# Optimization experiments

Hardware: AMD Instinct MI355X
Metric: run time of the kernel (lower is better)

## Reference

```python
import jax, jax.numpy as jnp
import numpy as np

N_NODES = 50000
N_EDGES = 1600000
IN_DIM = 128
HEADS = 8
OUT_C = 16  # per-head channels; HEADS*OUT_C == IN_DIM -> residual active
NEG_SLOPE = 0.2
BN_EPS = 1e-5


def setup_inputs() -> dict:
    key = jax.random.key(0)
    ks = jax.random.split(key, 8)
    x = jax.random.normal(ks[0], (N_NODES, IN_DIM), dtype=jnp.float32)
    edge_index = jax.random.randint(ks[1], (2, N_EDGES), 0, N_NODES, dtype=jnp.int64)
    # GATConv params (PyG: shared lin for src/dst on single-tensor input)
    W = jax.random.normal(ks[2], (IN_DIM, HEADS * OUT_C), dtype=jnp.float32) / np.sqrt(IN_DIM)
    att_src = jax.random.normal(ks[3], (HEADS, OUT_C), dtype=jnp.float32) / np.sqrt(OUT_C)
    att_dst = jax.random.normal(ks[4], (HEADS, OUT_C), dtype=jnp.float32) / np.sqrt(OUT_C)
    bias = jnp.zeros((HEADS * OUT_C,), dtype=jnp.float32)
    # BatchNorm1d affine params
    gamma = jnp.ones((HEADS * OUT_C,), dtype=jnp.float32)
    beta = jnp.zeros((HEADS * OUT_C,), dtype=jnp.float32)
    return {"x": x, "edge_index": edge_index, "W": W, "att_src": att_src,
            "att_dst": att_dst, "bias": bias, "gamma": gamma, "beta": beta}


def reference(x, edge_index, W, att_src, att_dst, bias, gamma, beta):
    N = x.shape[0]
    H, C = att_src.shape
    src, dst = edge_index[0], edge_index[1]

    xl = (x @ W).reshape(N, H, C)                      # [N,H,C]
    a_src = jnp.sum(xl * att_src[None], axis=-1)       # [N,H]
    a_dst = jnp.sum(xl * att_dst[None], axis=-1)       # [N,H]

    e = jax.nn.leaky_relu(a_src[src] + a_dst[dst], NEG_SLOPE)  # [E,H]
    # segment softmax over incoming edges of each dst node
    m = jax.ops.segment_max(e, dst, num_segments=N)    # [N,H], -inf for empty
    m = jnp.where(jnp.isfinite(m), m, 0.0)
    ex = jnp.exp(e - m[dst])                           # [E,H]
    denom = jax.ops.segment_sum(ex, dst, num_segments=N)
    alpha = ex / (denom[dst] + 1e-16)                  # [E,H]

    out = jax.ops.segment_sum(alpha[:, :, None] * xl[src], dst, num_segments=N)  # [N,H,C]
    h = out.reshape(N, H * C) + bias

    # BatchNorm1d (training mode: batch statistics, biased variance)
    mean = jnp.mean(h, axis=0)
    var = jnp.mean((h - mean) ** 2, axis=0)
    h = (h - mean) * jax.lax.rsqrt(var + BN_EPS) * gamma + beta

    h = jax.nn.relu(h)
    return x + h  # residual (in_dim == H*C)
```

## Files before the change

kernel.cpp:

```cpp
#include <hip/hip_runtime.h>
#include <hip/hip_fp16.h>
#include <math.h>

#define N_NODES 50000
#define N_EDGES 1600000
#define DIM 128
#define HEADS 8
#define NEG_SLOPE 0.2f
#define BN_EPS 1e-5f

typedef _Float16 f16x8 __attribute__((ext_vector_type(8)));
typedef float f32x4 __attribute__((ext_vector_type(4)));

#define NBUCK 196
#define SEGCAP 12288
#define CHUNK 8192
#define NB_A ((N_EDGES + CHUNK - 1) / CHUNK)
#define LIN_NB ((N_NODES + 127) / 128)
#define LIN_K1 195
#define LIN_K2 (LIN_NB - LIN_K1)
#define P1_NB (NB_A + LIN_K1)
#define P2_NB (NBUCK + LIN_K2)

struct BinAShm {
    int hist[NBUCK], excl[NBUCK], cnt2[NBUCK];
    int sc[256];
    unsigned int buf[CHUNK];
};
struct BinBShm {
    int la[256], ea[256];
    int hist[256], excl[256], cnt2[256], sc[256];
    unsigned short out[SEGCAP];
};
struct LinShm { __half wh[16384]; };

__device__ __forceinline__ void lin_block(
        int linb, const float* __restrict__ x, const float* __restrict__ W,
        const float* __restrict__ att_s, const float* __restrict__ att_d,
        __half* __restrict__ xlh, float* __restrict__ a_src,
        float* __restrict__ a_dst, __half* wh) {
    const int t = threadIdx.x;
    for (int v = t; v < 2048; v += 512) {
        const int g = v >> 6, lane = v & 63;
        const int nt = g >> 2, kt = g & 3;
        const int q = lane >> 4, n = lane & 15;
        #pragma unroll
        for (int j = 0; j < 8; ++j)
            wh[(size_t)(g * 64 + lane) * 8 + j] =
                __float2half(W[(kt * 32 + q * 8 + j) * DIM + nt * 16 + n]);
    }
    __syncthreads();

    const int wave = t >> 6;
    const int lane = t & 63;
    const int q = lane >> 4, n = lane & 15;
    const int nb = (linb * 8 + wave) * 16;

    const int rowA = min(nb + n, N_NODES - 1);
    const float* xr = x + (size_t)rowA * DIM;
    f16x8 a[4];
    #pragma unroll
    for (int kt = 0; kt < 4; ++kt) {
        const float4 p0 = *(const float4*)(xr + kt * 32 + q * 8);
        const float4 p1 = *(const float4*)(xr + kt * 32 + q * 8 + 4);
        a[kt][0] = (_Float16)p0.x; a[kt][1] = (_Float16)p0.y;
        a[kt][2] = (_Float16)p0.z; a[kt][3] = (_Float16)p0.w;
        a[kt][4] = (_Float16)p1.x; a[kt][5] = (_Float16)p1.y;
        a[kt][6] = (_Float16)p1.z; a[kt][7] = (_Float16)p1.w;
    }

    f32x4 acc[8];
    #pragma unroll
    for (int nt = 0; nt < 8; ++nt) acc[nt] = (f32x4){0.f, 0.f, 0.f, 0.f};

    const f16x8* wb = (const f16x8*)wh;
    #pragma unroll
    for (int nt = 0; nt < 8; ++nt) {
        #pragma unroll
        for (int kt = 0; kt < 4; ++kt) {
            const f16x8 b = wb[(nt * 4 + kt) * 64 + lane];
            acc[nt] = __builtin_amdgcn_mfma_f32_16x16x32_f16(a[kt], b, acc[nt], 0, 0, 0);
        }
    }

    const int r0 = nb + q * 4;
    #pragma unroll
    for (int nt = 0; nt < 8; ++nt) {
        const float as = att_s[nt * 16 + n];
        const float ad = att_d[nt * 16 + n];
        #pragma unroll
        for (int r = 0; r < 4; ++r) {
            const int row = r0 + r;
            const float v = acc[nt][r];
            float s = v * as;
            float d = v * ad;
            #pragma unroll
            for (int off = 8; off; off >>= 1) {
                s += __shfl_xor(s, off, 16);
                d += __shfl_xor(d, off, 16);
            }
            if (row < N_NODES) {
                xlh[(size_t)row * DIM + nt * 16 + n] = __float2half(v);
                if (n == 0) {
                    a_src[row * HEADS + nt] = s * 1.44269504f;
                    a_dst[row * HEADS + nt] = d * 1.44269504f;
                }
            }
        }
    }
}

__global__ __launch_bounds__(512) void k_phase1(
        const float* __restrict__ x, const float* __restrict__ W,
        const float* __restrict__ att_s, const float* __restrict__ att_d,
        const int* __restrict__ ei, unsigned int* __restrict__ meta,
        unsigned int* __restrict__ pairs, __half* __restrict__ xlh,
        float* __restrict__ a_src, float* __restrict__ a_dst) {
    __shared__ union { BinAShm a; LinShm l; } sh;
    const int t = threadIdx.x;

    if (blockIdx.x < NB_A) {
        const int blk = blockIdx.x;
        const int base = blk * CHUNK;
        const int cnt = min(CHUNK, N_EDGES - base);

        if (t < NBUCK) { sh.a.hist[t] = 0; sh.a.cnt2[t] = 0; }
        __syncthreads();
        for (int i = t * 4; i < cnt; i += 2048) {
            const int4 dv = *(const int4*)(ei + N_EDGES + base + i);
            atomicAdd(&sh.a.hist[dv.x >> 8], 1);
            atomicAdd(&sh.a.hist[dv.y >> 8], 1);
            atomicAdd(&sh.a.hist[dv.z >> 8], 1);
            atomicAdd(&sh.a.hist[dv.w >> 8], 1);
        }
        __syncthreads();
        if (t < 256) sh.a.sc[t] = (t < NBUCK) ? sh.a.hist[t] : 0;
        __syncthreads();
        for (int d = 1; d < 256; d <<= 1) {
            int xo = 0;
            if (t < 256 && t >= d) xo = sh.a.sc[t - d];
            __syncthreads();
            if (t < 256) sh.a.sc[t] += xo;
            __syncthreads();
        }
        if (t < NBUCK) {
            const int ex = sh.a.sc[t] - sh.a.hist[t];
            sh.a.excl[t] = ex;
            meta[(size_t)blk * NBUCK + t] =
                (unsigned int)sh.a.hist[t] | ((unsigned int)ex << 16);
        }
        __syncthreads();
        for (int i = t * 4; i < cnt; i += 2048) {
            const int4 sv = *(const int4*)(ei + base + i);
            const int4 dv = *(const int4*)(ei + N_EDGES + base + i);
            const int ss[4] = {sv.x, sv.y, sv.z, sv.w};
            const int dd[4] = {dv.x, dv.y, dv.z, dv.w};
            #pragma unroll
            for (int k = 0; k < 4; ++k) {
                const int b = dd[k] >> 8;
                const int r = atomicAdd(&sh.a.cnt2[b], 1);
                sh.a.buf[sh.a.excl[b] + r] = (unsigned int)ss[k]
                    | ((unsigned int)(dd[k] & 255) << 16);
            }
        }
        __syncthreads();
        for (int i = t * 4; i < cnt; i += 2048)
            *(int4*)(pairs + base + i) = *(const int4*)(sh.a.buf + i);
    } else {
        lin_block(blockIdx.x - NB_A, x, W, att_s, att_d, xlh, a_src, a_dst, sh.l.wh);
    }
}

__global__ __launch_bounds__(512) void k_phase2(
        const unsigned int* __restrict__ pairs, const unsigned int* __restrict__ meta,
        unsigned short* __restrict__ csr, int2* __restrict__ nrange,
        float* __restrict__ gsums,
        const float* __restrict__ x, const float* __restrict__ W,
        const float* __restrict__ att_s, const float* __restrict__ att_d,
        __half* __restrict__ xlh, float* __restrict__ a_src,
        float* __restrict__ a_dst) {
    __shared__ union { BinBShm b; LinShm l; } sh;
    const int t = threadIdx.x;

    if (blockIdx.x < NBUCK) {
        const int b = blockIdx.x;
        if (b == 0 && t < 256) gsums[t] = 0.f;

        if (t < 256) {
            int len = 0, off = 0;
            if (t < NB_A) {
                const unsigned int m = meta[(size_t)t * NBUCK + b];
                len = (int)(m & 0xFFFF);
                off = (int)(m >> 16);
            }
            sh.b.la[t] = len; sh.b.ea[t] = off;
            sh.b.hist[t] = 0; sh.b.cnt2[t] = 0;
        }
        __syncthreads();

        const int wave = t >> 6, lane = t & 63;

        for (int r = wave; r < NB_A; r += 8) {
            const int len = sh.b.la[r];
            const unsigned int* src = pairs + (size_t)r * CHUNK + sh.b.ea[r];
            for (int j = lane; j < len; j += 64)
                atomicAdd(&sh.b.hist[(src[j] >> 16) & 255], 1);
        }
        __syncthreads();
        if (t < 256) sh.b.sc[t] = sh.b.hist[t];
        __syncthreads();
        for (int d = 1; d < 256; d <<= 1) {
            int xo = 0;
            if (t < 256 && t >= d) xo = sh.b.sc[t - d];
            __syncthreads();
            if (t < 256) sh.b.sc[t] += xo;
            __syncthreads();
        }
        if (t < 256) {
            sh.b.excl[t] = sh.b.sc[t] - sh.b.hist[t];
            const int node = (b << 8) + t;
            if (node < N_NODES) {
                int2 rg;
                rg.x = b * SEGCAP + sh.b.excl[t];
                rg.y = rg.x + sh.b.hist[t];
                nrange[node] = rg;
            }
        }
        __syncthreads();
        const int cnt = sh.b.sc[255];

        for (int r = wave; r < NB_A; r += 8) {
            const int len = sh.b.la[r];
            const unsigned int* src = pairs + (size_t)r * CHUNK + sh.b.ea[r];
            for (int j = lane; j < len; j += 64) {
                const unsigned int u = src[j];
                const int dl = (u >> 16) & 255;
                const int p = atomicAdd(&sh.b.cnt2[dl], 1);
                sh.b.out[sh.b.excl[dl] + p] = (unsigned short)(u & 0xFFFF);
            }
        }
        __syncthreads();
        for (int i = t; i < cnt; i += 512)
            csr[(size_t)b * SEGCAP + i] = sh.b.out[i];
    } else {
        lin_block(LIN_K1 + (int)blockIdx.x - NBUCK, x, W, att_s, att_d,
                  xlh, a_src, a_dst, sh.l.wh);
    }
}

#define AGG_NB (N_NODES / 4)

__global__ void k_aggr9(const int2* __restrict__ nrange,
                        const unsigned short* __restrict__ csr,
                        const float* __restrict__ a_src, const float* __restrict__ a_dst,
                        const __half* __restrict__ xlh, float* __restrict__ y) {
    const int d = blockIdx.x * 4 + (threadIdx.x >> 6);
    const int lane = threadIdx.x & 63;
    const int g = lane >> 4;
    const int cl = lane & 15;
    const int h = cl >> 1;
    const int2 rg = nrange[d];
    const int lo = rg.x, hi = rg.y;
    const float ad = a_dst[d * HEADS + h];

    float acc[8];
    #pragma unroll
    for (int k = 0; k < 8; ++k) acc[k] = 0.f;
    float dsum = 0.f;

    int i = lo;
    for (; i + 16 <= hi; i += 16) {
        const int s0 = csr[i + g];
        const int s1 = csr[i + 4 + g];
        const int s2 = csr[i + 8 + g];
        const int s3 = csr[i + 12 + g];
        const float as0 = a_src[s0 * HEADS + h];
        const float as1 = a_src[s1 * HEADS + h];
        const float as2 = a_src[s2 * HEADS + h];
        const float as3 = a_src[s3 * HEADS + h];
        const f16x8 x0 = *(const f16x8*)(xlh + (size_t)s0 * DIM + cl * 8);
        const f16x8 x1 = *(const f16x8*)(xlh + (size_t)s1 * DIM + cl * 8);
        const f16x8 x2 = *(const f16x8*)(xlh + (size_t)s2 * DIM + cl * 8);
        const f16x8 x3 = *(const f16x8*)(xlh + (size_t)s3 * DIM + cl * 8);
        const float e0 = as0 + ad;
        const float e1 = as1 + ad;
        const float e2 = as2 + ad;
        const float e3 = as3 + ad;
        const float w0 = exp2f(fmaxf(e0, NEG_SLOPE * e0));
        const float w1 = exp2f(fmaxf(e1, NEG_SLOPE * e1));
        const float w2 = exp2f(fmaxf(e2, NEG_SLOPE * e2));
        const float w3 = exp2f(fmaxf(e3, NEG_SLOPE * e3));
        dsum += (w0 + w1) + (w2 + w3);
        #pragma unroll
        for (int k = 0; k < 8; ++k) acc[k] = fmaf(w0, (float)x0[k], acc[k]);
        #pragma unroll
        for (int k = 0; k < 8; ++k) acc[k] = fmaf(w1, (float)x1[k], acc[k]);
        #pragma unroll
        for (int k = 0; k < 8; ++k) acc[k] = fmaf(w2, (float)x2[k], acc[k]);
        #pragma unroll
        for (int k = 0; k < 8; ++k) acc[k] = fmaf(w3, (float)x3[k], acc[k]);
    }
    for (; i + 8 <= hi; i += 8) {
        const int s0 = csr[i + g];
        const int s1 = csr[i + 4 + g];
        const float as0 = a_src[s0 * HEADS + h];
        const float as1 = a_src[s1 * HEADS + h];
        const f16x8 x0 = *(const f16x8*)(xlh + (size_t)s0 * DIM + cl * 8);
        const f16x8 x1 = *(const f16x8*)(xlh + (size_t)s1 * DIM + cl * 8);
        const float e0 = as0 + ad;
        const float e1 = as1 + ad;
        const float w0 = exp2f(fmaxf(e0, NEG_SLOPE * e0));
        const float w1 = exp2f(fmaxf(e1, NEG_SLOPE * e1));
        dsum += w0 + w1;
        #pragma unroll
        for (int k = 0; k < 8; ++k) acc[k] = fmaf(w0, (float)x0[k], acc[k]);
        #pragma unroll
        for (int k = 0; k < 8; ++k) acc[k] = fmaf(w1, (float)x1[k], acc[k]);
    }
    for (; i < hi; i += 4) {
        const int idx = i + g;
        const int sv = csr[min(idx, hi - 1)];
        const float e = a_src[sv * HEADS + h] + ad;
        const f16x8 xv = *(const f16x8*)(xlh + (size_t)sv * DIM + cl * 8);
        float w = exp2f(fmaxf(e, NEG_SLOPE * e));
        if (idx >= hi) w = 0.f;
        dsum += w;
        #pragma unroll
        for (int k = 0; k < 8; ++k) acc[k] = fmaf(w, (float)xv[k], acc[k]);
    }
    #pragma unroll
    for (int k = 0; k < 8; ++k) {
        acc[k] += __shfl_xor(acc[k], 16);
        acc[k] += __shfl_xor(acc[k], 32);
    }
    dsum += __shfl_xor(dsum, 16);
    dsum += __shfl_xor(dsum, 32);
    const float inv = 1.f / (dsum + 1e-16f);
    float2 o;
    o.x = acc[2 * g] * inv;
    o.y = acc[2 * g + 1] * inv;
    *(float2*)(y + (size_t)d * DIM + cl * 8 + g * 2) = o;
}

__global__ void k_stats(const float* __restrict__ y, const float* __restrict__ bias,
                        float* __restrict__ gsums) {
    const int c = threadIdx.x;
    const float b = bias[c];
    float s = 0.f, ss = 0.f;
    for (int n = blockIdx.x; n < N_NODES; n += gridDim.x) {
        const float h = y[n * DIM + c] + b;
        s += h;
        ss += h * h;
    }
    atomicAdd(&gsums[c], s);
    atomicAdd(&gsums[DIM + c], ss);
}

__global__ void k_final(float* __restrict__ y, const float* __restrict__ x,
                        const float* __restrict__ sums, const float* __restrict__ sumsq,
                        const float* __restrict__ gamma, const float* __restrict__ beta,
                        const float* __restrict__ bias) {
    const int q = blockIdx.x * blockDim.x + threadIdx.x;
    const int cq = q & (DIM / 4 - 1);
    const float4 sm = ((const float4*)sums)[cq];
    const float4 sq = ((const float4*)sumsq)[cq];
    const float4 gm = ((const float4*)gamma)[cq];
    const float4 bt = ((const float4*)beta)[cq];
    const float4 bs = ((const float4*)bias)[cq];
    float4 v = ((const float4*)y)[q];
    const float4 xv = ((const float4*)x)[q];
    const float inv_n = 1.f / (float)N_NODES;
#define BNC(c) { const float mean = sm.c * inv_n;                         \
                 const float var = sq.c * inv_n - mean * mean;            \
                 const float sc = rsqrtf(var + BN_EPS) * gm.c;            \
                 const float sh = bt.c + (bs.c - mean) * sc;              \
                 v.c = xv.c + fmaxf(v.c * sc + sh, 0.f); }
    BNC(x) BNC(y) BNC(z) BNC(w)
#undef BNC
    ((float4*)y)[q] = v;
}

extern "C" void kernel_launch(void* const* d_in, const int* in_sizes, int n_in,
                              void* d_out, int out_size, void* d_ws, size_t ws_size,
                              hipStream_t stream) {
    const float* x     = (const float*)d_in[0];
    const int*   ei    = (const int*)  d_in[1];
    const float* W     = (const float*)d_in[2];
    const float* att_s = (const float*)d_in[3];
    const float* att_d = (const float*)d_in[4];
    const float* bias  = (const float*)d_in[5];
    const float* gamma = (const float*)d_in[6];
    const float* beta  = (const float*)d_in[7];
    float* y = (float*)d_out;

    __half* xlh  = (__half*)d_ws;
    float* a_src = (float*)(xlh + (size_t)N_NODES * DIM);
    float* a_dst = a_src + (size_t)N_NODES * HEADS;
    float* sums  = a_dst + (size_t)N_NODES * HEADS;
    float* sumsq = sums  + DIM;
    int2*  nrange = (int2*)(sumsq + DIM);
    unsigned int* meta  = (unsigned int*)(nrange + N_NODES);
    unsigned int* pairs = meta + (size_t)NB_A * NBUCK;
    unsigned short* csr = (unsigned short*)(pairs + (size_t)NB_A * CHUNK);

    k_phase1<<<P1_NB, 512, 0, stream>>>(x, W, att_s, att_d, ei, meta, pairs,
                                        xlh, a_src, a_dst);
    k_phase2<<<P2_NB, 512, 0, stream>>>(pairs, meta, csr, nrange, sums,
                                        x, W, att_s, att_d, xlh, a_src, a_dst);
    k_aggr9<<<AGG_NB, 256, 0, stream>>>(nrange, csr, a_src, a_dst, xlh, y);
    k_stats<<<512, DIM, 0, stream>>>(y, bias, sums);
    k_final<<<(size_t)N_NODES * DIM / 4 / 256, 256, 0, stream>>>(y, x, sums, sumsq,
                                                                 gamma, beta, bias);
}
```

Baseline: 234.1 us.

## Fuse second-pass binning with aggregation into one kernel using 128-node buckets

```diff
diff --git a/kernel.cpp b/kernel.cpp
--- a/kernel.cpp
+++ b/kernel.cpp
@@ -12,25 +12,17 @@
 typedef _Float16 f16x8 __attribute__((ext_vector_type(8)));
 typedef float f32x4 __attribute__((ext_vector_type(4)));
 
-#define NBUCK 196
-#define SEGCAP 12288
+#define NBUCK 391
+#define BSEGCAP 4864
 #define CHUNK 8192
 #define NB_A ((N_EDGES + CHUNK - 1) / CHUNK)
 #define LIN_NB ((N_NODES + 127) / 128)
-#define LIN_K1 195
-#define LIN_K2 (LIN_NB - LIN_K1)
-#define P1_NB (NB_A + LIN_K1)
-#define P2_NB (NBUCK + LIN_K2)
+#define P1_NB (NB_A + LIN_NB)
 
 struct BinAShm {
     int hist[NBUCK], excl[NBUCK], cnt2[NBUCK];
-    int sc[256];
+    int sc[512];
     unsigned int buf[CHUNK];
-};
-struct BinBShm {
-    int la[256], ea[256];
-    int hist[256], excl[256], cnt2[256], sc[256];
-    unsigned short out[SEGCAP];
 };
 struct LinShm { __half wh[16384]; };
 
@@ -124,23 +116,23 @@
         const int base = blk * CHUNK;
         const int cnt = min(CHUNK, N_EDGES - base);
 
-        if (t < NBUCK) { sh.a.hist[t] = 0; sh.a.cnt2[t] = 0; }
+        for (int j = t; j < NBUCK; j += 512) { sh.a.hist[j] = 0; sh.a.cnt2[j] = 0; }
         __syncthreads();
         for (int i = t * 4; i < cnt; i += 2048) {
             const int4 dv = *(const int4*)(ei + N_EDGES + base + i);
-            atomicAdd(&sh.a.hist[dv.x >> 8], 1);
-            atomicAdd(&sh.a.hist[dv.y >> 8], 1);
-            atomicAdd(&sh.a.hist[dv.z >> 8], 1);
-            atomicAdd(&sh.a.hist[dv.w >> 8], 1);
-        }
-        __syncthreads();
-        if (t < 256) sh.a.sc[t] = (t < NBUCK) ? sh.a.hist[t] : 0;
-        __syncthreads();
-        for (int d = 1; d < 256; d <<= 1) {
+            atomicAdd(&sh.a.hist[dv.x >> 7], 1);
+            atomicAdd(&sh.a.hist[dv.y >> 7], 1);
+            atomicAdd(&sh.a.hist[dv.z >> 7], 1);
+            atomicAdd(&sh.a.hist[dv.w >> 7], 1);
+        }
+        __syncthreads();
+        sh.a.sc[t] = (t < NBUCK) ? sh.a.hist[t] : 0;
+        __syncthreads();
+        for (int d = 1; d < 512; d <<= 1) {
             int xo = 0;
-            if (t < 256 && t >= d) xo = sh.a.sc[t - d];
+            if (t >= d) xo = sh.a.sc[t - d];
             __syncthreads();
-            if (t < 256) sh.a.sc[t] += xo;
+            sh.a.sc[t] += xo;
             __syncthreads();
         }
         if (t < NBUCK) {
@@ -157,10 +149,10 @@
             const int dd[4] = {dv.x, dv.y, dv.z, dv.w};
             #pragma unroll
             for (int k = 0; k < 4; ++k) {
-                const int b = dd[k] >> 8;
+                const int b = dd[k] >> 7;
                 const int r = atomicAdd(&sh.a.cnt2[b], 1);
                 sh.a.buf[sh.a.excl[b] + r] = (unsigned int)ss[k]
-                    | ((unsigned int)(dd[k] & 255) << 16);
+                    | ((unsigned int)(dd[k] & 127) << 16);
             }
         }
         __syncthreads();
@@ -171,175 +163,149 @@
     }
 }
 
-__global__ __launch_bounds__(512) void k_phase2(
+__global__ __launch_bounds__(1024) void k_binaggr(
         const unsigned int* __restrict__ pairs, const unsigned int* __restrict__ meta,
-        unsigned short* __restrict__ csr, int2* __restrict__ nrange,
-        float* __restrict__ gsums,
-        const float* __restrict__ x, const float* __restrict__ W,
-        const float* __restrict__ att_s, const float* __restrict__ att_d,
-        __half* __restrict__ xlh, float* __restrict__ a_src,
-        float* __restrict__ a_dst) {
-    __shared__ union { BinBShm b; LinShm l; } sh;
+        const float* __restrict__ a_src, const float* __restrict__ a_dst,
+        const __half* __restrict__ xlh, float* __restrict__ y,
+        float* __restrict__ gsums) {
+    __shared__ int la[NB_A], ea[NB_A];
+    __shared__ int hist[128], excl[128], cnt2[128], sc[128];
+    __shared__ unsigned short out[BSEGCAP];
     const int t = threadIdx.x;
-
-    if (blockIdx.x < NBUCK) {
-        const int b = blockIdx.x;
-        if (b == 0 && t < 256) gsums[t] = 0.f;
-
-        if (t < 256) {
-            int len = 0, off = 0;
-            if (t < NB_A) {
-                const unsigned int m = meta[(size_t)t * NBUCK + b];
-                len = (int)(m & 0xFFFF);
-                off = (int)(m >> 16);
-            }
-            sh.b.la[t] = len; sh.b.ea[t] = off;
-            sh.b.hist[t] = 0; sh.b.cnt2[t] = 0;
-        }
-        __syncthreads();
-
-        const int wave = t >> 6, lane = t & 63;
-
-        for (int r = wave; r < NB_A; r += 8) {
-            const int len = sh.b.la[r];
-            const unsigned int* src = pairs + (size_t)r * CHUNK + sh.b.ea[r];
-            for (int j = lane; j < len; j += 64)
-                atomicAdd(&sh.b.hist[(src[j] >> 16) & 255], 1);
-        }
-        __syncthreads();
-        if (t < 256) sh.b.sc[t] = sh.b.hist[t];
-        __syncthreads();
-        for (int d = 1; d < 256; d <<= 1) {
-            int xo = 0;
-            if (t < 256 && t >= d) xo = sh.b.sc[t - d];
-            __syncthreads();
-            if (t < 256) sh.b.sc[t] += xo;
-            __syncthreads();
-        }
-        if (t < 256) {
-            sh.b.excl[t] = sh.b.sc[t] - sh.b.hist[t];
-            const int node = (b << 8) + t;
-            if (node < N_NODES) {
-                int2 rg;
-                rg.x = b * SEGCAP + sh.b.excl[t];
-                rg.y = rg.x + sh.b.hist[t];
-                nrange[node] = rg;
-            }
-        }
-        __syncthreads();
-        const int cnt = sh.b.sc[255];
-
-        for (int r = wave; r < NB_A; r += 8) {
-            const int len = sh.b.la[r];
-            const unsigned int* src = pairs + (size_t)r * CHUNK + sh.b.ea[r];
-            for (int j = lane; j < len; j += 64) {
-                const unsigned int u = src[j];
-                const int dl = (u >> 16) & 255;
-                const int p = atomicAdd(&sh.b.cnt2[dl], 1);
-                sh.b.out[sh.b.excl[dl] + p] = (unsigned short)(u & 0xFFFF);
-            }
-        }
-        __syncthreads();
-        for (int i = t; i < cnt; i += 512)
-            csr[(size_t)b * SEGCAP + i] = sh.b.out[i];
-    } else {
-        lin_block(LIN_K1 + (int)blockIdx.x - NBUCK, x, W, att_s, att_d,
-                  xlh, a_src, a_dst, sh.l.wh);
-    }
-}
-
-#define AGG_NB (N_NODES / 4)
-
-__global__ void k_aggr9(const int2* __restrict__ nrange,
-                        const unsigned short* __restrict__ csr,
-                        const float* __restrict__ a_src, const float* __restrict__ a_dst,
-                        const __half* __restrict__ xlh, float* __restrict__ y) {
-    const int d = blockIdx.x * 4 + (threadIdx.x >> 6);
-    const int lane = threadIdx.x & 63;
+    const int b = blockIdx.x;
+    if (b == 0 && t < 256) gsums[t] = 0.f;
+
+    if (t < NB_A) {
+        const unsigned int m = meta[(size_t)t * NBUCK + b];
+        la[t] = (int)(m & 0xFFFF);
+        ea[t] = (int)(m >> 16);
+    }
+    if (t < 128) { hist[t] = 0; cnt2[t] = 0; }
+    __syncthreads();
+
+    const int wave = t >> 6, lane = t & 63;
+
+    for (int r = wave; r < NB_A; r += 16) {
+        const int len = la[r];
+        const unsigned int* src = pairs + (size_t)r * CHUNK + ea[r];
+        for (int j = lane; j < len; j += 64)
+            atomicAdd(&hist[(src[j] >> 16) & 127], 1);
+    }
+    __syncthreads();
+    if (t < 128) sc[t] = hist[t];
+    __syncthreads();
+    for (int d = 1; d < 128; d <<= 1) {
+        int xo = 0;
+        if (t < 128 && t >= d) xo = sc[t - d];
+        __syncthreads();
+        if (t < 128) sc[t] += xo;
+        __syncthreads();
+    }
+    if (t < 128) excl[t] = sc[t] - hist[t];
+    __syncthreads();
+
+    for (int r = wave; r < NB_A; r += 16) {
+        const int len = la[r];
+        const unsigned int* src = pairs + (size_t)r * CHUNK + ea[r];
+        for (int j = lane; j < len; j += 64) {
+            const unsigned int u = src[j];
+            const int dl = (u >> 16) & 127;
+            const int p = atomicAdd(&cnt2[dl], 1);
+            out[excl[dl] + p] = (unsigned short)(u & 0xFFFF);
+        }
+    }
+    __syncthreads();
+
     const int g = lane >> 4;
     const int cl = lane & 15;
     const int h = cl >> 1;
-    const int2 rg = nrange[d];
-    const int lo = rg.x, hi = rg.y;
-    const float ad = a_dst[d * HEADS + h];
-
-    float acc[8];
-    #pragma unroll
-    for (int k = 0; k < 8; ++k) acc[k] = 0.f;
-    float dsum = 0.f;
-
-    int i = lo;
-    for (; i + 16 <= hi; i += 16) {
-        const int s0 = csr[i + g];
-        const int s1 = csr[i + 4 + g];
-        const int s2 = csr[i + 8 + g];
-        const int s3 = csr[i + 12 + g];
-        const float as0 = a_src[s0 * HEADS + h];
-        const float as1 = a_src[s1 * HEADS + h];
-        const float as2 = a_src[s2 * HEADS + h];
-        const float as3 = a_src[s3 * HEADS + h];
-        const f16x8 x0 = *(const f16x8*)(xlh + (size_t)s0 * DIM + cl * 8);
-        const f16x8 x1 = *(const f16x8*)(xlh + (size_t)s1 * DIM + cl * 8);
-        const f16x8 x2 = *(const f16x8*)(xlh + (size_t)s2 * DIM + cl * 8);
-        const f16x8 x3 = *(const f16x8*)(xlh + (size_t)s3 * DIM + cl * 8);
-        const float e0 = as0 + ad;
-        const float e1 = as1 + ad;
-        const float e2 = as2 + ad;
-        const float e3 = as3 + ad;
-        const float w0 = exp2f(fmaxf(e0, NEG_SLOPE * e0));
-        const float w1 = exp2f(fmaxf(e1, NEG_SLOPE * e1));
-        const float w2 = exp2f(fmaxf(e2, NEG_SLOPE * e2));
-        const float w3 = exp2f(fmaxf(e3, NEG_SLOPE * e3));
-        dsum += (w0 + w1) + (w2 + w3);
-        #pragma unroll
-        for (int k = 0; k < 8; ++k) acc[k] = fmaf(w0, (float)x0[k], acc[k]);
-        #pragma unroll
-        for (int k = 0; k < 8; ++k) acc[k] = fmaf(w1, (float)x1[k], acc[k]);
-        #pragma unroll
-        for (int k = 0; k < 8; ++k) acc[k] = fmaf(w2, (float)x2[k], acc[k]);
-        #pragma unroll
-        for (int k = 0; k < 8; ++k) acc[k] = fmaf(w3, (float)x3[k], acc[k]);
-    }
-    for (; i + 8 <= hi; i += 8) {
-        const int s0 = csr[i + g];
-        const int s1 = csr[i + 4 + g];
-        const float as0 = a_src[s0 * HEADS + h];
-        const float as1 = a_src[s1 * HEADS + h];
-        const f16x8 x0 = *(const f16x8*)(xlh + (size_t)s0 * DIM + cl * 8);
-        const f16x8 x1 = *(const f16x8*)(xlh + (size_t)s1 * DIM + cl * 8);
-        const float e0 = as0 + ad;
-        const float e1 = as1 + ad;
-        const float w0 = exp2f(fmaxf(e0, NEG_SLOPE * e0));
-        const float w1 = exp2f(fmaxf(e1, NEG_SLOPE * e1));
-        dsum += w0 + w1;
-        #pragma unroll
-        for (int k = 0; k < 8; ++k) acc[k] = fmaf(w0, (float)x0[k], acc[k]);
-        #pragma unroll
-        for (int k = 0; k < 8; ++k) acc[k] = fmaf(w1, (float)x1[k], acc[k]);
-    }
-    for (; i < hi; i += 4) {
-        const int idx = i + g;
-        const int sv = csr[min(idx, hi - 1)];
-        const float e = a_src[sv * HEADS + h] + ad;
-        const f16x8 xv = *(const f16x8*)(xlh + (size_t)sv * DIM + cl * 8);
-        float w = exp2f(fmaxf(e, NEG_SLOPE * e));
-        if (idx >= hi) w = 0.f;
-        dsum += w;
-        #pragma unroll
-        for (int k = 0; k < 8; ++k) acc[k] = fmaf(w, (float)xv[k], acc[k]);
-    }
-    #pragma unroll
+
     for (int k = 0; k < 8; ++k) {
-        acc[k] += __shfl_xor(acc[k], 16);
-        acc[k] += __shfl_xor(acc[k], 32);
-    }
-    dsum += __shfl_xor(dsum, 16);
-    dsum += __shfl_xor(dsum, 32);
-    const float inv = 1.f / (dsum + 1e-16f);
-    float2 o;
-    o.x = acc[2 * g] * inv;
-    o.y = acc[2 * g + 1] * inv;
-    *(float2*)(y + (size_t)d * DIM + cl * 8 + g * 2) = o;
+        const int nl = k * 16 + wave;
+        const int d = (b << 7) + nl;
+        if (d >= N_NODES) continue;
+        const int lo = excl[nl];
+        const int hi = lo + hist[nl];
+        const float ad = a_dst[d * HEADS + h];
+
+        float acc[8];
+        #pragma unroll
+        for (int q = 0; q < 8; ++q) acc[q] = 0.f;
+        float dsum = 0.f;
+
+        int i = lo;
+        for (; i + 16 <= hi; i += 16) {
+            const int s0 = out[i + g];
+            const int s1 = out[i + 4 + g];
+            const int s2 = out[i + 8 + g];
+            const int s3 = out[i + 12 + g];
+            const float as0 = a_src[s0 * HEADS + h];
+            const float as1 = a_src[s1 * HEADS + h];
+            const float as2 = a_src[s2 * HEADS + h];
+            const float as3 = a_src[s3 * HEADS + h];
+            const f16x8 x0 = *(const f16x8*)(xlh + (size_t)s0 * DIM + cl * 8);
+            const f16x8 x1 = *(const f16x8*)(xlh + (size_t)s1 * DIM + cl * 8);
+            const f16x8 x2 = *(const f16x8*)(xlh + (size_t)s2 * DIM + cl * 8);
+            const f16x8 x3 = *(const f16x8*)(xlh + (size_t)s3 * DIM + cl * 8);
+            const float e0 = as0 + ad;
+            const float e1 = as1 + ad;
+            const float e2 = as2 + ad;
+            const float e3 = as3 + ad;
+            const float w0 = exp2f(fmaxf(e0, NEG_SLOPE * e0));
+            const float w1 = exp2f(fmaxf(e1, NEG_SLOPE * e1));
+            const float w2 = exp2f(fmaxf(e2, NEG_SLOPE * e2));
+            const float w3 = exp2f(fmaxf(e3, NEG_SLOPE * e3));
+            dsum += (w0 + w1) + (w2 + w3);
+            #pragma unroll
+            for (int q = 0; q < 8; ++q) acc[q] = fmaf(w0, (float)x0[q], acc[q]);
+            #pragma unroll
+            for (int q = 0; q < 8; ++q) acc[q] = fmaf(w1, (float)x1[q], acc[q]);
+            #pragma unroll
+            for (int q = 0; q < 8; ++q) acc[q] = fmaf(w2, (float)x2[q], acc[q]);
+            #pragma unroll
+            for (int q = 0; q < 8; ++q) acc[q] = fmaf(w3, (float)x3[q], acc[q]);
+        }
+        for (; i + 8 <= hi; i += 8) {
+            const int s0 = out[i + g];
+            const int s1 = out[i + 4 + g];
+            const float as0 = a_src[s0 * HEADS + h];
+            const float as1 = a_src[s1 * HEADS + h];
+            const f16x8 x0 = *(const f16x8*)(xlh + (size_t)s0 * DIM + cl * 8);
+            const f16x8 x1 = *(const f16x8*)(xlh + (size_t)s1 * DIM + cl * 8);
+            const float e0 = as0 + ad;
+            const float e1 = as1 + ad;
+            const float w0 = exp2f(fmaxf(e0, NEG_SLOPE * e0));
+            const float w1 = exp2f(fmaxf(e1, NEG_SLOPE * e1));
+            dsum += w0 + w1;
+            #pragma unroll
+            for (int q = 0; q < 8; ++q) acc[q] = fmaf(w0, (float)x0[q], acc[q]);
+            #pragma unroll
+            for (int q = 0; q < 8; ++q) acc[q] = fmaf(w1, (float)x1[q], acc[q]);
+        }
+        for (; i < hi; i += 4) {
+            const int idx = i + g;
+            const int sv = out[min(idx, hi - 1)];
+            const float e = a_src[sv * HEADS + h] + ad;
+            const f16x8 xv = *(const f16x8*)(xlh + (size_t)sv * DIM + cl * 8);
+            float w = exp2f(fmaxf(e, NEG_SLOPE * e));
+            if (idx >= hi) w = 0.f;
+            dsum += w;
+            #pragma unroll
+            for (int q = 0; q < 8; ++q) acc[q] = fmaf(w, (float)xv[q], acc[q]);
+        }
+        #pragma unroll
+        for (int q = 0; q < 8; ++q) {
+            acc[q] += __shfl_xor(acc[q], 16);
+            acc[q] += __shfl_xor(acc[q], 32);
+        }
+        dsum += __shfl_xor(dsum, 16);
+        dsum += __shfl_xor(dsum, 32);
+        const float inv = 1.f / (dsum + 1e-16f);
+        float2 o;
+        o.x = acc[2 * g] * inv;
+        o.y = acc[2 * g + 1] * inv;
+        *(float2*)(y + (size_t)d * DIM + cl * 8 + g * 2) = o;
+    }
 }
 
 __global__ void k_stats(const float* __restrict__ y, const float* __restrict__ bias,
@@ -398,16 +364,12 @@
     float* a_dst = a_src + (size_t)N_NODES * HEADS;
     float* sums  = a_dst + (size_t)N_NODES * HEADS;
     float* sumsq = sums  + DIM;
-    int2*  nrange = (int2*)(sumsq + DIM);
-    unsigned int* meta  = (unsigned int*)(nrange + N_NODES);
+    unsigned int* meta  = (unsigned int*)(sumsq + DIM);
     unsigned int* pairs = meta + (size_t)NB_A * NBUCK;
-    unsigned short* csr = (unsigned short*)(pairs + (size_t)NB_A * CHUNK);
 
     k_phase1<<<P1_NB, 512, 0, stream>>>(x, W, att_s, att_d, ei, meta, pairs,
                                         xlh, a_src, a_dst);
-    k_phase2<<<P2_NB, 512, 0, stream>>>(pairs, meta, csr, nrange, sums,
-                                        x, W, att_s, att_d, xlh, a_src, a_dst);
-    k_aggr9<<<AGG_NB, 256, 0, stream>>>(nrange, csr, a_src, a_dst, xlh, y);
+    k_binaggr<<<NBUCK, 1024, 0, stream>>>(pairs, meta, a_src, a_dst, xlh, y, sums);
     k_stats<<<512, DIM, 0, stream>>>(y, bias, sums);
     k_final<<<(size_t)N_NODES * DIM / 4 / 256, 256, 0, stream>>>(y, x, sums, sumsq,
                                                                  gamma, beta, bias);
```

After: 239.2 us. 1.02x slower.
